# Performance work log

Measured on AMD Instinct MI355X. Metric: run time of the kernel, lower is better.

Reference implementation:

```python
import math
import jax, jax.numpy as jnp
import numpy as np

SR = 44100
N_HARMONICS = 64
EPS = 1e-5
LOG10 = math.log(10.0)


def scale_function(x):
    # ddsp_pytorch util.scale_function: 2 * sigmoid(x)**log(10) + 1e-7
    return 2.0 * jax.nn.sigmoid(x) ** LOG10 + 1e-7


def setup_inputs() -> dict:
    key = jax.random.key(0)
    k1, k2, k3 = jax.random.split(key, 3)
    bs, n_samples = 32, 64000
    # f0 in [80, 480] Hz so upper harmonics cross Nyquist for some frames
    f0_hz = jax.random.uniform(k1, (bs, n_samples), dtype=jnp.float32) * 400.0 + 80.0
    harmonic_amplitudes = jax.random.normal(k2, (bs, n_samples, N_HARMONICS + 1), dtype=jnp.float32)
    phase = jax.random.uniform(k3, (bs,), dtype=jnp.float32) * 2.0 * jnp.pi
    return {"f0_hz": f0_hz, "harmonic_amplitudes": harmonic_amplitudes, "phase": phase}


def reference(f0_hz, harmonic_amplitudes, phase):
    ha = scale_function(harmonic_amplitudes)            # (bs, S, H+1)
    f0 = f0_hz[..., None]                               # (bs, S, 1)
    total_amplitude = ha[..., :1]                       # (bs, S, 1)
    ha = ha[..., 1:]                                    # (bs, S, H)
    harm = jnp.arange(1, N_HARMONICS + 1, dtype=f0.dtype)  # (H,)
    # anti-alias: zero harmonics above Nyquist
    aa = (f0 * harm < SR / 2).astype(f0.dtype)
    ha_aa = ha * aa
    ha_aa = ha_aa / (jnp.sum(ha_aa, axis=-1, keepdims=True) + EPS)
    ha_aa = ha_aa * total_amplitude
    # phase integration
    omega = jnp.cumsum(2.0 * jnp.pi * f0 / SR, axis=1)  # (bs, S, 1)
    omega = omega + phase.reshape(-1, 1, 1)
    omegas = omega * harm                               # (bs, S, H)
    signal = jnp.sum(jnp.sin(omegas) * ha_aa, axis=-1)  # (bs, S)
    return signal
```

## Files before the change

### kernel.cpp

```cpp
#include <hip/hip_runtime.h>
#include <math.h>

#define BATCH    32
#define CHUNK    128
#define NCHUNK   500
#define TAB_N    1152

__device__ __forceinline__ float scale_fn(float x) {
    float e = exp2f(-1.4426950408889634f * x);
    float l = log2f(1.0f + e);
    return 2.0f * exp2f(-2.302585092994046f * l) + 1e-7f;
}

__global__ __launch_bounds__(128) void table_kernel(float* __restrict__ gtab) {
    int i = blockIdx.x * 128 + threadIdx.x;
    if (i < TAB_N) gtab[i] = scale_fn(fmaf((float)i, 0.015625f, -8.0f));
}

__global__ __launch_bounds__(128) void chunk_sum_kernel(
        const float* __restrict__ f0, double* __restrict__ csum) {
    int bx = blockIdx.x;
    int t  = threadIdx.x;
    double v = (double)f0[(long)bx * CHUNK + t];
    for (int off = 32; off > 0; off >>= 1) v += __shfl_down(v, off, 64);
    __shared__ double ws[2];
    if ((t & 63) == 0) ws[t >> 6] = v;
    __syncthreads();
    if (t == 0) csum[bx] = ws[0] + ws[1];
}

__global__ __launch_bounds__(512) void chunk_scan_kernel(double* __restrict__ csum) {
    int r = blockIdx.x;
    int t = threadIdx.x;
    int lane = t & 63, w = t >> 6;
    double orig = (t < NCHUNK) ? csum[(long)r * NCHUNK + t] : 0.0;
    double v = orig;
    for (int off = 1; off < 64; off <<= 1) {
        double n = __shfl_up(v, off, 64);
        if (lane >= off) v += n;
    }
    __shared__ double wsum[8];
    if (lane == 63) wsum[w] = v;
    __syncthreads();
    double add = 0.0;
    for (int i = 0; i < w; ++i) add += wsum[i];
    v += add;
    if (t < NCHUNK) csum[(long)r * NCHUNK + t] = v - orig;
}

__global__ __launch_bounds__(512, 4) void osc_kernel(
        const float* __restrict__ f0,
        const float* __restrict__ ha,
        const float* __restrict__ phase,
        const double* __restrict__ csum,
        const float* __restrict__ gtab,
        float* __restrict__ out) {
    int bx = blockIdx.x;
    int r  = bx / NCHUNK;
    int t  = threadIdx.x;
    int lane = t & 63, w = t >> 6;

    long sbase = (long)bx * CHUNK;
    const float* hablk = ha + sbase * 65;

    __shared__ float  amp[CHUNK * 65];
    __shared__ float  tab[TAB_N];
    __shared__ float  f0s[CHUNK];
    __shared__ float  nuA[CHUNK];
    __shared__ double wsum[2];

    if (t < 288) ((float4*)tab)[t] = ((const float4*)gtab)[t];
    if (t < 32)  ((float4*)f0s)[t] = ((const float4*)(f0 + sbase))[t];
    {
        const float4* src = (const float4*)hablk;
        float4* dst = (float4*)amp;
        #pragma unroll
        for (int i = 0; i < 4; ++i)
            dst[i * 512 + t] = src[i * 512 + t];
        if (t < 32) dst[2048 + t] = src[2048 + t];
    }
    __syncthreads();

    double v = 0.0;
    if (t < 128) {
        v = (double)f0s[t];
        for (int off = 1; off < 64; off <<= 1) {
            double n = __shfl_up(v, off, 64);
            if (lane >= off) v += n;
        }
        if (lane == 63) wsum[w] = v;
    }
    __syncthreads();
    if (t < 128) {
        if (w == 1) v += wsum[0];
        v += csum[bx];
        double x = v * (1.0 / 44100.0) + (double)phase[r] * 0.15915494309189535;
        x -= floor(x);
        nuA[t] = (float)x;
    }
    __syncthreads();

    int s  = w * 16 + (lane & 15);
    int q  = lane >> 4;
    int h0 = q * 16;

    float f0v = f0s[s];
    float nu  = nuA[s];

    float k0 = floorf(22050.0f / f0v);
    if (f0v * (k0 + 1.0f) < 22050.0f)      k0 += 1.0f;
    else if (!(f0v * k0 < 22050.0f))       k0 -= 1.0f;

    float c2;
    {
        float th = 6.283185307179586f * nu;
        c2 = 2.0f * __cosf(th);
    }
    float m1 = (float)(h0 + 1) * nu; m1 -= floorf(m1);
    float m2 = (float)(h0 + 2) * nu; m2 -= floorf(m2);
    float sA = __sinf(6.283185307179586f * m1);
    float sB = 6.283185307179586f * m2;  sB = __sinf(sB);

    const float* arow = amp + s * 65 + 1 + h0;

    float S1 = 0.0f, S2 = 0.0f;
    #pragma unroll
    for (int j = 0; j < 16; j += 2) {
        float a0 = arow[j];
        float a1 = arow[j + 1];
        float tc0 = fmaf(a0, 64.0f, 512.0f);
        tc0 = fminf(fmaxf(tc0, 0.0f), 1022.99f);
        float fi0 = floorf(tc0); int i0 = (int)fi0; float fr0 = tc0 - fi0;
        float w0 = fmaf(fr0, tab[i0 + 1] - tab[i0], tab[i0]);
        float tc1 = fmaf(a1, 64.0f, 512.0f);
        tc1 = fminf(fmaxf(tc1, 0.0f), 1022.99f);
        float fi1 = floorf(tc1); int i1 = (int)fi1; float fr1 = tc1 - fi1;
        float w1 = fmaf(fr1, tab[i1 + 1] - tab[i1], tab[i1]);

        w0 = ((float)(h0 + 1 + j) <= k0) ? w0 : 0.0f;
        w1 = ((float)(h0 + 2 + j) <= k0) ? w1 : 0.0f;

        S1 += w0; S2 = fmaf(w0, sA, S2);
        S1 += w1; S2 = fmaf(w1, sB, S2);

        float sn1 = fmaf(c2, sB, -sA);
        float sn2 = fmaf(c2, sn1, -sB);
        sA = sn1; sB = sn2;
    }

    S1 += __shfl_xor(S1, 16, 64);
    S1 += __shfl_xor(S1, 32, 64);
    S2 += __shfl_xor(S2, 16, 64);
    S2 += __shfl_xor(S2, 32, 64);

    if (q == 0) {
        float total = scale_fn(amp[s * 65]);
        out[sbase + s] = total * S2 / (S1 + 1e-5f);
    }
}

extern "C" void kernel_launch(void* const* d_in, const int* in_sizes, int n_in,
                              void* d_out, int out_size, void* d_ws, size_t ws_size,
                              hipStream_t stream) {
    (void)in_sizes; (void)n_in; (void)out_size; (void)ws_size;
    const float* f0    = (const float*)d_in[0];
    const float* ha    = (const float*)d_in[1];
    const float* phase = (const float*)d_in[2];
    float* out = (float*)d_out;

    double* csum = (double*)d_ws;
    float*  gtab = (float*)((char*)d_ws + 131072);

    table_kernel<<<(TAB_N + 127) / 128, 128, 0, stream>>>(gtab);
    chunk_sum_kernel<<<BATCH * NCHUNK, CHUNK, 0, stream>>>(f0, csum);
    chunk_scan_kernel<<<BATCH, 512, 0, stream>>>(csum);
    osc_kernel<<<BATCH * NCHUNK, 512, 0, stream>>>(f0, ha, phase, csum, gtab, out);
}
```

Measured before the change: 692.4 us.

## Make oscillator kernel persistent with double-buffered async global-to-LDS loads

Moves the per-sample phase computation into a separate nu_kernel that writes phases to a workspace array. The oscillator kernel becomes persistent with 512 blocks. Each block loops over chunks and prefetches the next chunk's amplitudes into a second LDS buffer via global_load_lds while computing the current one. The aim is to overlap the memory-bound amplitude load with compute and cut block launch overhead, at the cost of an extra kernel launch, an extra phase array round-trip, doubled LDS use that may lower occupancy, and fewer resident blocks.

```diff
diff --git a/kernel.cpp b/kernel.cpp
--- a/kernel.cpp
+++ b/kernel.cpp
@@ -4,13 +4,19 @@
 #define BATCH    32
 #define CHUNK    128
 #define NCHUNK   500
+#define NCH_TOT  (BATCH * NCHUNK)
 #define TAB_N    1152
+#define PBLOCKS  512
 
 __device__ __forceinline__ float scale_fn(float x) {
     float e = exp2f(-1.4426950408889634f * x);
     float l = log2f(1.0f + e);
     return 2.0f * exp2f(-2.302585092994046f * l) + 1e-7f;
 }
+
+#define GLOAD_LDS16(g, l)  __builtin_amdgcn_global_load_lds(                 \
+    (const __attribute__((address_space(1))) void*)(g),                      \
+    (__attribute__((address_space(3))) void*)(l), 16, 0, 0)
 
 __global__ __launch_bounds__(128) void table_kernel(float* __restrict__ gtab) {
     int i = blockIdx.x * 128 + threadIdx.x;
@@ -48,114 +54,126 @@
     if (t < NCHUNK) csum[(long)r * NCHUNK + t] = v - orig;
 }
 
-__global__ __launch_bounds__(512, 4) void osc_kernel(
-        const float* __restrict__ f0,
-        const float* __restrict__ ha,
-        const float* __restrict__ phase,
-        const double* __restrict__ csum,
-        const float* __restrict__ gtab,
-        float* __restrict__ out) {
+__global__ __launch_bounds__(128) void nu_kernel(
+        const float* __restrict__ f0, const double* __restrict__ csum,
+        const float* __restrict__ phase, float* __restrict__ nuarr) {
     int bx = blockIdx.x;
     int r  = bx / NCHUNK;
     int t  = threadIdx.x;
     int lane = t & 63, w = t >> 6;
+    long sbase = (long)bx * CHUNK;
+    double v = (double)f0[sbase + t];
+    for (int off = 1; off < 64; off <<= 1) {
+        double n = __shfl_up(v, off, 64);
+        if (lane >= off) v += n;
+    }
+    __shared__ double wsum[2];
+    if (lane == 63) wsum[w] = v;
+    __syncthreads();
+    if (w == 1) v += wsum[0];
+    v += csum[bx];
+    double x = v * (1.0 / 44100.0) + (double)phase[r] * 0.15915494309189535;
+    x -= floor(x);
+    nuarr[sbase + t] = (float)x;
+}
 
-    long sbase = (long)bx * CHUNK;
-    const float* hablk = ha + sbase * 65;
+__global__ __launch_bounds__(512, 4) void osc_kernel(
+        const float* __restrict__ f0,
+        const float* __restrict__ ha,
+        const float* __restrict__ nuarr,
+        const float* __restrict__ gtab,
+        float* __restrict__ out) {
+    int b = blockIdx.x;
+    int t = threadIdx.x;
+    int lane = t & 63, w = t >> 6;
 
-    __shared__ float  amp[CHUNK * 65];
-    __shared__ float  tab[TAB_N];
-    __shared__ float  f0s[CHUNK];
-    __shared__ float  nuA[CHUNK];
-    __shared__ double wsum[2];
+    __shared__ float slab[2][CHUNK * 65];
+    __shared__ float tab[TAB_N];
 
     if (t < 288) ((float4*)tab)[t] = ((const float4*)gtab)[t];
-    if (t < 32)  ((float4*)f0s)[t] = ((const float4*)(f0 + sbase))[t];
-    {
-        const float4* src = (const float4*)hablk;
-        float4* dst = (float4*)amp;
+
+    int nIter = (b < (NCH_TOT - 31 * PBLOCKS)) ? 32 : 31;
+
+    auto stage = [&](int buf, int c) {
+        const char* src = (const char*)ha + (long)c * (CHUNK * 65 * 4);
+        char*       dst = (char*)slab[buf];
         #pragma unroll
-        for (int i = 0; i < 4; ++i)
-            dst[i * 512 + t] = src[i * 512 + t];
-        if (t < 32) dst[2048 + t] = src[2048 + t];
-    }
-    __syncthreads();
+        for (int k = 0; k < 4; ++k) {
+            int rr = w + 8 * k;
+            GLOAD_LDS16(src + rr * 1024 + lane * 16,
+                        dst + rr * 1024 + lane * 16);
+        }
+        if (w == 0)
+            GLOAD_LDS16(src + 32256 + lane * 16,
+                        dst + 32256 + lane * 16);
+    };
 
-    double v = 0.0;
-    if (t < 128) {
-        v = (double)f0s[t];
-        for (int off = 1; off < 64; off <<= 1) {
-            double n = __shfl_up(v, off, 64);
-            if (lane >= off) v += n;
+    stage(0, b);
+
+    for (int i = 0; i < nIter; ++i) {
+        int c = i * PBLOCKS + b;
+        __syncthreads();
+        if (i + 1 < nIter) stage((i + 1) & 1, c + PBLOCKS);
+
+        const float* amp = slab[i & 1];
+        long sbase = (long)c * CHUNK;
+        int s  = w * 16 + (lane & 15);
+        int q  = lane >> 4;
+        int h0 = q * 16;
+
+        float f0v = f0[sbase + s];
+        float nu  = nuarr[sbase + s];
+
+        float k0 = floorf(22050.0f / f0v);
+        if (f0v * (k0 + 1.0f) < 22050.0f)      k0 += 1.0f;
+        else if (!(f0v * k0 < 22050.0f))       k0 -= 1.0f;
+
+        float c2;
+        {
+            float th = 6.283185307179586f * nu;
+            c2 = 2.0f * __cosf(th);
         }
-        if (lane == 63) wsum[w] = v;
-    }
-    __syncthreads();
-    if (t < 128) {
-        if (w == 1) v += wsum[0];
-        v += csum[bx];
-        double x = v * (1.0 / 44100.0) + (double)phase[r] * 0.15915494309189535;
-        x -= floor(x);
-        nuA[t] = (float)x;
-    }
-    __syncthreads();
+        float m1 = (float)(h0 + 1) * nu; m1 -= floorf(m1);
+        float m2 = (float)(h0 + 2) * nu; m2 -= floorf(m2);
+        float sA = __sinf(6.283185307179586f * m1);
+        float sB = __sinf(6.283185307179586f * m2);
 
-    int s  = w * 16 + (lane & 15);
-    int q  = lane >> 4;
-    int h0 = q * 16;
+        const float* arow = amp + s * 65 + 1 + h0;
 
-    float f0v = f0s[s];
-    float nu  = nuA[s];
+        float S1 = 0.0f, S2 = 0.0f;
+        #pragma unroll
+        for (int j = 0; j < 16; j += 2) {
+            float a0 = arow[j];
+            float a1 = arow[j + 1];
+            float tc0 = fmaf(a0, 64.0f, 512.0f);
+            tc0 = fminf(fmaxf(tc0, 0.0f), 1022.99f);
+            float fi0 = floorf(tc0); int i0 = (int)fi0; float fr0 = tc0 - fi0;
+            float w0 = fmaf(fr0, tab[i0 + 1] - tab[i0], tab[i0]);
+            float tc1 = fmaf(a1, 64.0f, 512.0f);
+            tc1 = fminf(fmaxf(tc1, 0.0f), 1022.99f);
+            float fi1 = floorf(tc1); int i1 = (int)fi1; float fr1 = tc1 - fi1;
+            float w1 = fmaf(fr1, tab[i1 + 1] - tab[i1], tab[i1]);
 
-    float k0 = floorf(22050.0f / f0v);
-    if (f0v * (k0 + 1.0f) < 22050.0f)      k0 += 1.0f;
-    else if (!(f0v * k0 < 22050.0f))       k0 -= 1.0f;
+            w0 = ((float)(h0 + 1 + j) <= k0) ? w0 : 0.0f;
+            w1 = ((float)(h0 + 2 + j) <= k0) ? w1 : 0.0f;
 
-    float c2;
-    {
-        float th = 6.283185307179586f * nu;
-        c2 = 2.0f * __cosf(th);
-    }
-    float m1 = (float)(h0 + 1) * nu; m1 -= floorf(m1);
-    float m2 = (float)(h0 + 2) * nu; m2 -= floorf(m2);
-    float sA = __sinf(6.283185307179586f * m1);
-    float sB = 6.283185307179586f * m2;  sB = __sinf(sB);
+            S1 += w0; S2 = fmaf(w0, sA, S2);
+            S1 += w1; S2 = fmaf(w1, sB, S2);
 
-    const float* arow = amp + s * 65 + 1 + h0;
+            float sn1 = fmaf(c2, sB, -sA);
+            float sn2 = fmaf(c2, sn1, -sB);
+            sA = sn1; sB = sn2;
+        }
 
-    float S1 = 0.0f, S2 = 0.0f;
-    #pragma unroll
-    for (int j = 0; j < 16; j += 2) {
-        float a0 = arow[j];
-        float a1 = arow[j + 1];
-        float tc0 = fmaf(a0, 64.0f, 512.0f);
-        tc0 = fminf(fmaxf(tc0, 0.0f), 1022.99f);
-        float fi0 = floorf(tc0); int i0 = (int)fi0; float fr0 = tc0 - fi0;
-        float w0 = fmaf(fr0, tab[i0 + 1] - tab[i0], tab[i0]);
-        float tc1 = fmaf(a1, 64.0f, 512.0f);
-        tc1 = fminf(fmaxf(tc1, 0.0f), 1022.99f);
-        float fi1 = floorf(tc1); int i1 = (int)fi1; float fr1 = tc1 - fi1;
-        float w1 = fmaf(fr1, tab[i1 + 1] - tab[i1], tab[i1]);
+        S1 += __shfl_xor(S1, 16, 64);
+        S1 += __shfl_xor(S1, 32, 64);
+        S2 += __shfl_xor(S2, 16, 64);
+        S2 += __shfl_xor(S2, 32, 64);
 
-        w0 = ((float)(h0 + 1 + j) <= k0) ? w0 : 0.0f;
-        w1 = ((float)(h0 + 2 + j) <= k0) ? w1 : 0.0f;
-
-        S1 += w0; S2 = fmaf(w0, sA, S2);
-        S1 += w1; S2 = fmaf(w1, sB, S2);
-
-        float sn1 = fmaf(c2, sB, -sA);
-        float sn2 = fmaf(c2, sn1, -sB);
-        sA = sn1; sB = sn2;
-    }
-
-    S1 += __shfl_xor(S1, 16, 64);
-    S1 += __shfl_xor(S1, 32, 64);
-    S2 += __shfl_xor(S2, 16, 64);
-    S2 += __shfl_xor(S2, 32, 64);
-
-    if (q == 0) {
-        float total = scale_fn(amp[s * 65]);
-        out[sbase + s] = total * S2 / (S1 + 1e-5f);
+        if (q == 0) {
+            float total = scale_fn(amp[s * 65]);
+            out[sbase + s] = total * S2 / (S1 + 1e-5f);
+        }
     }
 }
 
@@ -170,9 +188,11 @@
 
     double* csum = (double*)d_ws;
     float*  gtab = (float*)((char*)d_ws + 131072);
+    float*  nuarr = (float*)((char*)d_ws + 262144);
 
     table_kernel<<<(TAB_N + 127) / 128, 128, 0, stream>>>(gtab);
-    chunk_sum_kernel<<<BATCH * NCHUNK, CHUNK, 0, stream>>>(f0, csum);
+    chunk_sum_kernel<<<NCH_TOT, CHUNK, 0, stream>>>(f0, csum);
     chunk_scan_kernel<<<BATCH, 512, 0, stream>>>(csum);
-    osc_kernel<<<BATCH * NCHUNK, 512, 0, stream>>>(f0, ha, phase, csum, gtab, out);
+    nu_kernel<<<NCH_TOT, CHUNK, 0, stream>>>(f0, csum, phase, nuarr);
+    osc_kernel<<<PBLOCKS, 512, 0, stream>>>(f0, ha, nuarr, gtab, out);
 }
```

After: 678.6 us. 1.02x faster.
